# Optimization experiments

Hardware: AMD Instinct MI355X
Metric: run time of the kernel (lower is better)

Reference implementation:

```python
import jax, jax.numpy as jnp
import numpy as np

LOG_2PI = float(np.log(2.0 * np.pi))
N = 33554432  # 2**25


def setup_inputs() -> dict:
    key = jax.random.key(0)
    k1, k2, k3, k4 = jax.random.split(key, 4)
    return {
        "x": jax.random.normal(k1, (N,), dtype=jnp.float32),
        "log_sw": jax.random.normal(k2, (1,), dtype=jnp.float32),
        "log_sz": jax.random.normal(k3, (1,), dtype=jnp.float32),
        "log_sx": jax.random.normal(k4, (1,), dtype=jnp.float32),
    }


def reference(x, log_sw, log_sz, log_sx):
    # Covariance: b*J + a*I with b = sw^2, a = sz^2 + sx^2 (compound symmetric).
    # Closed-form MVN log_prob via Sherman-Morrison + matrix determinant lemma:
    #   Sigma^{-1} = I/a - (b/(a*(a+N*b))) * J
    #   logdet(Sigma) = (N-1)*log(a) + log(a + N*b)
    n = x.shape[0]
    b = jnp.exp(2.0 * log_sw[0])                      # sw^2
    a = jnp.exp(2.0 * log_sz[0]) + jnp.exp(2.0 * log_sx[0])  # sz^2 + sx^2
    s = jnp.sum(x)                                    # 1'x
    xx = jnp.dot(x, x)                                # x'x
    quad = xx / a - b * s * s / (a * (a + n * b))     # x' Sigma^{-1} x
    logdet = (n - 1) * jnp.log(a) + jnp.log(a + n * b)
    return -0.5 * (n * LOG_2PI + logdet + quad)
```

## Files before the change

kernel.cpp:

```cpp
#include <hip/hip_runtime.h>
#include <math.h>

#define NBLK 2048
#define NTHR 256
#define NWAVE (NTHR / 64)

__global__ __launch_bounds__(NTHR) void grt_partial_kernel(
    const float* __restrict__ x, float2* __restrict__ part, int n4) {
    const float4* __restrict__ x4 = reinterpret_cast<const float4*>(x);
    const int tid = blockIdx.x * NTHR + threadIdx.x;
    const int stride = NBLK * NTHR;

    float s0 = 0.f, s1 = 0.f, s2 = 0.f, s3 = 0.f;
    float q0 = 0.f, q1 = 0.f, q2 = 0.f, q3 = 0.f;
    int i = tid;
    for (; i + 3 * stride < n4; i += 4 * stride) {
        float4 a = x4[i];
        float4 b = x4[i + stride];
        float4 c = x4[i + 2 * stride];
        float4 d = x4[i + 3 * stride];
        s0 += a.x + a.y + a.z + a.w;
        s1 += b.x + b.y + b.z + b.w;
        s2 += c.x + c.y + c.z + c.w;
        s3 += d.x + d.y + d.z + d.w;
        q0 = fmaf(a.x, a.x, q0); q0 = fmaf(a.y, a.y, q0);
        q0 = fmaf(a.z, a.z, q0); q0 = fmaf(a.w, a.w, q0);
        q1 = fmaf(b.x, b.x, q1); q1 = fmaf(b.y, b.y, q1);
        q1 = fmaf(b.z, b.z, q1); q1 = fmaf(b.w, b.w, q1);
        q2 = fmaf(c.x, c.x, q2); q2 = fmaf(c.y, c.y, q2);
        q2 = fmaf(c.z, c.z, q2); q2 = fmaf(c.w, c.w, q2);
        q3 = fmaf(d.x, d.x, q3); q3 = fmaf(d.y, d.y, q3);
        q3 = fmaf(d.z, d.z, q3); q3 = fmaf(d.w, d.w, q3);
    }
    for (; i < n4; i += stride) {
        float4 a = x4[i];
        s0 += a.x + a.y + a.z + a.w;
        q0 = fmaf(a.x, a.x, q0); q0 = fmaf(a.y, a.y, q0);
        q0 = fmaf(a.z, a.z, q0); q0 = fmaf(a.w, a.w, q0);
    }
    float s = (s0 + s1) + (s2 + s3);
    float q = (q0 + q1) + (q2 + q3);

    #pragma unroll
    for (int off = 32; off > 0; off >>= 1) {
        s += __shfl_down(s, off, 64);
        q += __shfl_down(q, off, 64);
    }

    __shared__ float2 lds[NWAVE];
    const int lane = threadIdx.x & 63;
    const int wave = threadIdx.x >> 6;
    if (lane == 0) lds[wave] = make_float2(s, q);
    __syncthreads();

    if (threadIdx.x == 0) {
        float2 acc = lds[0];
        #pragma unroll
        for (int w = 1; w < NWAVE; ++w) {
            acc.x += lds[w].x;
            acc.y += lds[w].y;
        }
        part[blockIdx.x] = acc;
    }
}

__global__ __launch_bounds__(64) void grt_final_kernel(
    const float4* __restrict__ part4,
    const float* __restrict__ log_sw, const float* __restrict__ log_sz,
    const float* __restrict__ log_sx, float* __restrict__ out, float dn) {
    float s = 0.f, q = 0.f;
    #pragma unroll 4
    for (int i = threadIdx.x; i < NBLK / 2; i += 64) {
        float4 v = part4[i];
        s += v.x + v.z;
        q += v.y + v.w;
    }

    #pragma unroll
    for (int off = 32; off > 0; off >>= 1) {
        s += __shfl_down(s, off, 64);
        q += __shfl_down(q, off, 64);
    }

    if (threadIdx.x == 0) {
        double ss = (double)s, qq = (double)q;
        double n = (double)dn;
        double b = exp(2.0 * (double)log_sw[0]);
        double a = exp(2.0 * (double)log_sz[0]) + exp(2.0 * (double)log_sx[0]);
        double quad = qq / a - b * ss * ss / (a * (a + n * b));
        double logdet = (n - 1.0) * log(a) + log(a + n * b);
        const double LOG_2PI = 1.837877066409345483560659472811;
        out[0] = (float)(-0.5 * (n * LOG_2PI + logdet + quad));
    }
}

extern "C" void kernel_launch(void* const* d_in, const int* in_sizes, int n_in,
                              void* d_out, int out_size, void* d_ws, size_t ws_size,
                              hipStream_t stream) {
    const float* x      = (const float*)d_in[0];
    const float* log_sw = (const float*)d_in[1];
    const float* log_sz = (const float*)d_in[2];
    const float* log_sx = (const float*)d_in[3];
    float* out = (float*)d_out;
    int n = in_sizes[0];
    int n4 = n >> 2;

    float2* part = (float2*)d_ws;

    grt_partial_kernel<<<NBLK, NTHR, 0, stream>>>(x, part, n4);
    grt_final_kernel<<<1, 64, 0, stream>>>((const float4*)part, log_sw, log_sz,
                                           log_sx, out, (float)n);
}
```

Baseline: 29.62 us.

## Use block-contiguous fully unrolled loads with nontemporal hints in partial reduction

Adds a fast path for the case where the element count exactly matches grid size times 16 float4 per thread. In that path each block reads a contiguous chunk with a fully unrolled loop of 16 loads. All loads now use the nontemporal builtin, which hints that the streamed data should not be kept in cache. The aim is more memory requests in flight per thread and less loop overhead; the fixed-size path relies on n matching the compile-time constants, with a generic grid-stride fallback otherwise.

```diff
diff --git a/kernel.cpp b/kernel.cpp
--- a/kernel.cpp
+++ b/kernel.cpp
@@ -4,39 +4,47 @@
 #define NBLK 2048
 #define NTHR 256
 #define NWAVE (NTHR / 64)
+#define PER_THREAD 16
+
+typedef float f32x4 __attribute__((ext_vector_type(4)));
 
 __global__ __launch_bounds__(NTHR) void grt_partial_kernel(
     const float* __restrict__ x, float2* __restrict__ part, int n4) {
-    const float4* __restrict__ x4 = reinterpret_cast<const float4*>(x);
-    const int tid = blockIdx.x * NTHR + threadIdx.x;
-    const int stride = NBLK * NTHR;
+    const f32x4* __restrict__ x4 = reinterpret_cast<const f32x4*>(x);
 
     float s0 = 0.f, s1 = 0.f, s2 = 0.f, s3 = 0.f;
     float q0 = 0.f, q1 = 0.f, q2 = 0.f, q3 = 0.f;
-    int i = tid;
-    for (; i + 3 * stride < n4; i += 4 * stride) {
-        float4 a = x4[i];
-        float4 b = x4[i + stride];
-        float4 c = x4[i + 2 * stride];
-        float4 d = x4[i + 3 * stride];
-        s0 += a.x + a.y + a.z + a.w;
-        s1 += b.x + b.y + b.z + b.w;
-        s2 += c.x + c.y + c.z + c.w;
-        s3 += d.x + d.y + d.z + d.w;
-        q0 = fmaf(a.x, a.x, q0); q0 = fmaf(a.y, a.y, q0);
-        q0 = fmaf(a.z, a.z, q0); q0 = fmaf(a.w, a.w, q0);
-        q1 = fmaf(b.x, b.x, q1); q1 = fmaf(b.y, b.y, q1);
-        q1 = fmaf(b.z, b.z, q1); q1 = fmaf(b.w, b.w, q1);
-        q2 = fmaf(c.x, c.x, q2); q2 = fmaf(c.y, c.y, q2);
-        q2 = fmaf(c.z, c.z, q2); q2 = fmaf(c.w, c.w, q2);
-        q3 = fmaf(d.x, d.x, q3); q3 = fmaf(d.y, d.y, q3);
-        q3 = fmaf(d.z, d.z, q3); q3 = fmaf(d.w, d.w, q3);
-    }
-    for (; i < n4; i += stride) {
-        float4 a = x4[i];
-        s0 += a.x + a.y + a.z + a.w;
-        q0 = fmaf(a.x, a.x, q0); q0 = fmaf(a.y, a.y, q0);
-        q0 = fmaf(a.z, a.z, q0); q0 = fmaf(a.w, a.w, q0);
+
+    if (n4 == NBLK * NTHR * PER_THREAD) {
+        const int base = blockIdx.x * (NTHR * PER_THREAD) + threadIdx.x;
+        #pragma unroll
+        for (int g = 0; g < PER_THREAD / 4; ++g) {
+            f32x4 a = __builtin_nontemporal_load(&x4[base + (g * 4 + 0) * NTHR]);
+            f32x4 b = __builtin_nontemporal_load(&x4[base + (g * 4 + 1) * NTHR]);
+            f32x4 c = __builtin_nontemporal_load(&x4[base + (g * 4 + 2) * NTHR]);
+            f32x4 d = __builtin_nontemporal_load(&x4[base + (g * 4 + 3) * NTHR]);
+            s0 += a[0] + a[1] + a[2] + a[3];
+            s1 += b[0] + b[1] + b[2] + b[3];
+            s2 += c[0] + c[1] + c[2] + c[3];
+            s3 += d[0] + d[1] + d[2] + d[3];
+            q0 = fmaf(a[0], a[0], q0); q0 = fmaf(a[1], a[1], q0);
+            q0 = fmaf(a[2], a[2], q0); q0 = fmaf(a[3], a[3], q0);
+            q1 = fmaf(b[0], b[0], q1); q1 = fmaf(b[1], b[1], q1);
+            q1 = fmaf(b[2], b[2], q1); q1 = fmaf(b[3], b[3], q1);
+            q2 = fmaf(c[0], c[0], q2); q2 = fmaf(c[1], c[1], q2);
+            q2 = fmaf(c[2], c[2], q2); q2 = fmaf(c[3], c[3], q2);
+            q3 = fmaf(d[0], d[0], q3); q3 = fmaf(d[1], d[1], q3);
+            q3 = fmaf(d[2], d[2], q3); q3 = fmaf(d[3], d[3], q3);
+        }
+    } else {
+        const int tid = blockIdx.x * NTHR + threadIdx.x;
+        const int stride = NBLK * NTHR;
+        for (int i = tid; i < n4; i += stride) {
+            f32x4 a = __builtin_nontemporal_load(&x4[i]);
+            s0 += a[0] + a[1] + a[2] + a[3];
+            q0 = fmaf(a[0], a[0], q0); q0 = fmaf(a[1], a[1], q0);
+            q0 = fmaf(a[2], a[2], q0); q0 = fmaf(a[3], a[3], q0);
+        }
     }
     float s = (s0 + s1) + (s2 + s3);
     float q = (q0 + q1) + (q2 + q3);
```

After: 26.77 us (median of 2 runs). 9.6% less time.
